# Performance work log

Measured on AMD Instinct MI355X. Metric: run time of the kernel, lower is better.

## Reference

```python
import jax, jax.numpy as jnp
import numpy as np

N, E, H = 4096, 32768, 8
D0, C1, C2, C3 = 256, 448, 384, 256
K, M, G = 4, 500, 2000
NEG = 0.2   # GATConv LeakyReLU negative slope
EPS = 1e-5  # LayerNorm eps


def _gat(x, src, dst, W, a_s, a_d, b, heads, out_ch, concat):
    # PyG GATConv (self-loops already appended to src/dst by caller).
    n = x.shape[0]
    xp = (x @ W).reshape(n, heads, out_ch)                 # [N,H,C]
    s = jnp.einsum('nhc,hc->nh', xp, a_s)                  # alpha_src per node
    d = jnp.einsum('nhc,hc->nh', xp, a_d)                  # alpha_dst per node
    e = jax.nn.leaky_relu(s[src] + d[dst], NEG)            # [E,H]
    m = jax.ops.segment_max(e, dst, num_segments=n)
    m = jnp.where(jnp.isfinite(m), m, 0.0)
    p = jnp.exp(e - m[dst])
    z = jax.ops.segment_sum(p, dst, num_segments=n)
    alpha = p / (z[dst] + 1e-16)                           # per-dst softmax
    out = jax.ops.segment_sum(alpha[:, :, None] * xp[src], dst, num_segments=n)
    out = out.reshape(n, heads * out_ch) if concat else out[:, 0, :]
    return out + b


def _ln(x, g, b):
    mu = x.mean(-1, keepdims=True)
    v = ((x - mu) ** 2).mean(-1, keepdims=True)
    return (x - mu) * jax.lax.rsqrt(v + EPS) * g + b


def setup_inputs() -> dict:
    key = jax.random.key(0)
    ks = jax.random.split(key, 20)
    sc = 0.05
    inp = {
        'x': jax.random.normal(ks[0], (N, D0), jnp.float32),
        'edge_index': jax.random.randint(ks[1], (2, E), 0, N, jnp.int32),
        'W1': jax.random.normal(ks[2], (D0, H * C1), jnp.float32) * sc,
        'as1': jax.random.normal(ks[3], (H, C1), jnp.float32) * sc,
        'ad1': jax.random.normal(ks[4], (H, C1), jnp.float32) * sc,
        'b1': jnp.zeros((H * C1,), jnp.float32),
        'g1': jnp.ones((H * C1,), jnp.float32),
        'be1': jnp.zeros((H * C1,), jnp.float32),
        'W2': jax.random.normal(ks[5], (H * C1, H * C2), jnp.float32) * sc,
        'as2': jax.random.normal(ks[6], (H, C2), jnp.float32) * sc,
        'ad2': jax.random.normal(ks[7], (H, C2), jnp.float32) * sc,
        'b2': jnp.zeros((H * C2,), jnp.float32),
        'g2': jnp.ones((H * C2,), jnp.float32),
        'be2': jnp.zeros((H * C2,), jnp.float32),
        'W3': jax.random.normal(ks[8], (H * C2, H * C3), jnp.float32) * sc,
        'as3': jax.random.normal(ks[9], (H, C3), jnp.float32) * sc,
        'ad3': jax.random.normal(ks[10], (H, C3), jnp.float32) * sc,
        'b3': jnp.zeros((H * C3,), jnp.float32),
        'g3': jnp.ones((H * C3,), jnp.float32),
        'be3': jnp.zeros((H * C3,), jnp.float32),
        'Wh': jax.random.normal(ks[11], (K, H * C3, M), jnp.float32) * sc,
        'ash': jax.random.normal(ks[12], (K, 1, M), jnp.float32) * sc,
        'adh': jax.random.normal(ks[13], (K, 1, M), jnp.float32) * sc,
        'bh': jnp.zeros((K, M), jnp.float32),
        'idx': jnp.arange(G, dtype=jnp.int32).reshape(K, M),
    }
    return inp


def reference(x, edge_index, W1, as1, ad1, b1, g1, be1, W2, as2, ad2, b2, g2, be2,
              W3, as3, ad3, b3, g3, be3, Wh, ash, adh, bh, idx):
    n = x.shape[0]
    # eval mode: dropout_edge is identity; PyG GATConv adds self-loops
    loops = jnp.arange(n, dtype=edge_index.dtype)
    src = jnp.concatenate([edge_index[0], loops])
    dst = jnp.concatenate([edge_index[1], loops])

    h = jax.nn.relu(_gat(x, src, dst, W1, as1, ad1, b1, H, C1, True))
    h = _ln(h, g1, be1)
    h = jax.nn.relu(_gat(h, src, dst, W2, as2, ad2, b2, H, C2, True))
    h = _ln(h, g2, be2)
    h = jax.nn.relu(_gat(h, src, dst, W3, as3, ad3, b3, H, C3, True))
    h = _ln(h, g3, be3)

    per_head = jax.vmap(
        lambda Wk, ak_s, ak_d, bk: _gat(h, src, dst, Wk, ak_s, ak_d, bk, 1, M, False)
    )(Wh, ash, adh, bh)                                    # [K,N,M]

    vals = per_head.transpose(1, 0, 2).reshape(n, K * M)   # [N, G] in head order
    full = jnp.zeros((n, G), vals.dtype).at[:, idx.reshape(-1)].set(vals)
    return full, per_head
```

## Files before the change

kernel.cpp:

```cpp
#include <hip/hip_runtime.h>

#define NN 4096
#define EE 32768
#define ETOT (EE + NN)
#define HH 8
#define KK 4
#define MM 500
#define GG 2000
#define NEGS 0.2f
#define LNEPS 1e-5f

typedef unsigned short ushort;
typedef _Float16 half_t;
typedef __attribute__((ext_vector_type(8))) _Float16 half8;
typedef __attribute__((ext_vector_type(4))) float floatx4;


__device__ __forceinline__ void get_edge(const int* __restrict__ ei, int e, int& s, int& d) {
    if (e < EE) { s = ei[e]; d = ei[EE + e]; }
    else        { s = e - EE; d = e - EE; }
}

__device__ __forceinline__ half_t f2h(float x) { return (half_t)x; }

__device__ __forceinline__ void async_lds16(const half_t* g, half_t* l) {
    __builtin_amdgcn_global_load_lds(
        (const __attribute__((address_space(1))) unsigned int*)(const void*)g,
        (__attribute__((address_space(3))) unsigned int*)(void*)l,
        16, 0, 0);
}


__global__ void k_zero_i(int* p, int n) {
    int i = blockIdx.x * 256 + threadIdx.x;
    if (i < n) p[i] = 0;
}

__global__ void k_count(const int* __restrict__ ei, int* deg) {
    int e = blockIdx.x * 256 + threadIdx.x;
    if (e < ETOT) { int s, d; get_edge(ei, e, s, d); atomicAdd(&deg[d], 1); }
}

__global__ void k_scan(const int* __restrict__ deg, int* rs, int n) {
    __shared__ int sums[1024];
    int tid = threadIdx.x;
    int base = tid * 4;
    int loc[4]; int s = 0;
    #pragma unroll
    for (int i = 0; i < 4; i++) {
        int v = (base + i < n) ? deg[base + i] : 0;
        loc[i] = s; s += v;
    }
    sums[tid] = s;
    __syncthreads();
    for (int off = 1; off < 1024; off <<= 1) {
        int v = (tid >= off) ? sums[tid - off] : 0;
        __syncthreads();
        sums[tid] += v;
        __syncthreads();
    }
    int prev = (tid > 0) ? sums[tid - 1] : 0;
    #pragma unroll
    for (int i = 0; i < 4; i++)
        if (base + i < n) rs[base + i] = prev + loc[i];
    if (tid == 1023) rs[n] = sums[1023];
}

__global__ void k_fill(const int* __restrict__ ei, const int* __restrict__ rs,
                       int* cur, int* csr_src, int* csr_eid) {
    int e = blockIdx.x * 256 + threadIdx.x;
    if (e < ETOT) {
        int s, d; get_edge(ei, e, s, d);
        int pos = rs[d] + atomicAdd(&cur[d], 1);
        csr_src[pos] = s;
        csr_eid[pos] = e;
    }
}


__global__ void k_f2h(const float* __restrict__ in, half_t* __restrict__ out, int n) {
    int i = blockIdx.x * 256 + threadIdx.x;
    if (i < n) out[i] = f2h(in[i]);
}


__global__ __launch_bounds__(256) void k_wt(const float* __restrict__ W,
                                            half_t* __restrict__ Wt,
                                            int Kd, int Nvalid, int ldw,
                                            long long sW, long long sWt) {
    __shared__ float t[32][33];
    const float* Wp = W + (size_t)blockIdx.z * sW;
    half_t* Wtp = Wt + (size_t)blockIdx.z * sWt;
    int n0 = blockIdx.x * 32, k0 = blockIdx.y * 32;
    int tx = threadIdx.x & 31, ty = threadIdx.x >> 5;
    #pragma unroll
    for (int i = 0; i < 32; i += 8)
        t[ty + i][tx] = (n0 + tx < Nvalid) ? Wp[(size_t)(k0 + ty + i) * ldw + n0 + tx] : 0.f;
    __syncthreads();
    #pragma unroll
    for (int i = 0; i < 32; i += 8)
        Wtp[(size_t)(n0 + ty + i) * Kd + k0 + tx] = f2h(t[tx][ty + i]);
}


#define BM 128
#define BN 128
#define BK 64

__global__ __launch_bounds__(256) void k_gemm_mfma(
    const half_t* __restrict__ A,
    const half_t* __restrict__ Bt,
    half_t* __restrict__ C,
    int Kd, int Nreal, int ldc,
    long long strideBt, long long strideC)
{
    __shared__ __align__(16) half_t As[BM * BK];
    __shared__ __align__(16) half_t Bs[BN * BK];

    const half_t* Btp = Bt + (size_t)blockIdx.z * strideBt;
    half_t* Cp = C + (size_t)blockIdx.z * strideC;
    int col0 = blockIdx.x * BN, row0 = blockIdx.y * BM;

    int lane = threadIdx.x & 63;
    int wave = threadIdx.x >> 6;
    int wm = (wave >> 1) * 64, wn = (wave & 1) * 64;

    int srow = wave * 32 + (lane >> 3);
    int gchunk = (lane & 7) ^ ((lane >> 3) & 7);
    const half_t* ga = A   + (size_t)(row0 + srow) * Kd + gchunk * 8;
    const half_t* gb = Btp + (size_t)(col0 + srow) * Kd + gchunk * 8;
    half_t* lA = &As[(wave * 32) * BK];
    half_t* lB = &Bs[(wave * 32) * BK];

    int r = lane & 15;
    int rx = r & 7;

    floatx4 acc[4][4];
    #pragma unroll
    for (int i = 0; i < 4; i++)
        #pragma unroll
        for (int j = 0; j < 4; j++) acc[i][j] = (floatx4){0.f, 0.f, 0.f, 0.f};

    for (int k0 = 0; k0 < Kd; k0 += BK) {
        #pragma unroll
        for (int j = 0; j < 4; j++) {
            async_lds16(ga + k0 + (size_t)(j * 8) * Kd, lA + (j * 8) * BK);
            async_lds16(gb + k0 + (size_t)(j * 8) * Kd, lB + (j * 8) * BK);
        }
        __syncthreads();
        #pragma unroll
        for (int kk = 0; kk < BK; kk += 32) {
            int phys = (((kk >> 3) + (lane >> 4)) ^ rx) << 3;
            half8 a[4], b[4];
            #pragma unroll
            for (int i = 0; i < 4; i++)
                a[i] = *(const half8*)&As[(wm + i * 16 + r) * BK + phys];
            #pragma unroll
            for (int j = 0; j < 4; j++)
                b[j] = *(const half8*)&Bs[(wn + j * 16 + r) * BK + phys];
            #pragma unroll
            for (int i = 0; i < 4; i++)
                #pragma unroll
                for (int j = 0; j < 4; j++)
                    acc[i][j] = __builtin_amdgcn_mfma_f32_16x16x32_f16(a[i], b[j], acc[i][j], 0, 0, 0);
        }
        __syncthreads();
    }

    int q4 = (lane >> 4) * 4;
    #pragma unroll
    for (int i = 0; i < 4; i++) {
        #pragma unroll
        for (int rr = 0; rr < 4; rr++) {
            int row = row0 + wm + i * 16 + q4 + rr;
            #pragma unroll
            for (int j = 0; j < 4; j++) {
                int col = col0 + wn + j * 16 + (lane & 15);
                if (col < Nreal) Cp[(size_t)row * ldc + col] = f2h(acc[i][j][rr]);
            }
        }
    }
}


__global__ void k_sd(const half_t* __restrict__ xp, const float* __restrict__ as_,
                     const float* __restrict__ ad_, float* s, float* d, float* z,
                     int H, int C) {
    int n = blockIdx.x / H, h = blockIdx.x % H;
    int lane = threadIdx.x;
    const half_t* row = xp + (size_t)n * H * C + (size_t)h * C;
    const float* av = as_ + (size_t)h * C;
    const float* bv = ad_ + (size_t)h * C;
    float ss = 0.f, dd = 0.f;
    for (int c = lane; c < C; c += 64) {
        float x = (float)row[c];
        ss += x * av[c];
        dd += x * bv[c];
    }
    #pragma unroll
    for (int o = 32; o > 0; o >>= 1) {
        ss += __shfl_down(ss, o, 64);
        dd += __shfl_down(dd, o, 64);
    }
    if (lane == 0) { s[n * H + h] = ss; d[n * H + h] = dd; z[n * H + h] = 0.f; }
}


__global__ void k_edge(const int* __restrict__ ei, const float* __restrict__ s,
                       const float* __restrict__ d, float* ew, float* z,
                       int H, int total) {
    int i = blockIdx.x * 256 + threadIdx.x;
    if (i >= total) return;
    int e = i / H, h = i - e * H;
    int sn, dn; get_edge(ei, e, sn, dn);
    float v = s[sn * H + h] + d[dn * H + h];
    v = (v >= 0.f) ? v : NEGS * v;
    float p = expf(v);
    ew[i] = p;
    atomicAdd(&z[dn * H + h], p);
}


__global__ __launch_bounds__(256) void k_agg_ln(
    const half_t* __restrict__ xp, const float* __restrict__ p, const float* __restrict__ z,
    const int* __restrict__ csr_src, const int* __restrict__ csr_eid,
    const int* __restrict__ rs, const float* __restrict__ bias,
    const float* __restrict__ gam, const float* __restrict__ bet,
    half_t* __restrict__ outh, int H, int C) {
    __shared__ int sh_src[256];
    __shared__ int sh_eid[256];
    __shared__ float sh_w[256 * HH];
    __shared__ float red[256];
    __shared__ float red2[256];
    int n = blockIdx.x, tid = threadIdx.x;
    int Dout = H * C;
    int NCH = Dout >> 3;
    int CCH = C >> 3;
    int start = rs[n], end = rs[n + 1];
    float acc[2][8];
    #pragma unroll
    for (int a = 0; a < 2; a++)
        #pragma unroll
        for (int e = 0; e < 8; e++) acc[a][e] = 0.f;

    for (int e0 = start; e0 < end; e0 += 256) {
        int cnt = min(256, end - e0);
        if (tid < cnt) { sh_src[tid] = csr_src[e0 + tid]; sh_eid[tid] = csr_eid[e0 + tid]; }
        __syncthreads();
        for (int i = tid; i < cnt * H; i += 256)
            sh_w[i] = p[sh_eid[i / H] * H + (i % H)];
        __syncthreads();
        int ai = 0;
        for (int ch = tid; ch < NCH; ch += 256, ai++) {
            int h = ch / CCH;
            float a0 = acc[ai][0], a1 = acc[ai][1], a2 = acc[ai][2], a3 = acc[ai][3];
            float a4 = acc[ai][4], a5 = acc[ai][5], a6 = acc[ai][6], a7 = acc[ai][7];
            for (int i = 0; i < cnt; i++) {
                float w = sh_w[i * H + h];
                half8 v = *(const half8*)(xp + (size_t)sh_src[i] * Dout + (ch << 3));
                a0 += w * (float)v[0]; a1 += w * (float)v[1];
                a2 += w * (float)v[2]; a3 += w * (float)v[3];
                a4 += w * (float)v[4]; a5 += w * (float)v[5];
                a6 += w * (float)v[6]; a7 += w * (float)v[7];
            }
            acc[ai][0] = a0; acc[ai][1] = a1; acc[ai][2] = a2; acc[ai][3] = a3;
            acc[ai][4] = a4; acc[ai][5] = a5; acc[ai][6] = a6; acc[ai][7] = a7;
        }
        __syncthreads();
    }

    float vals[2][8];
    float sum = 0.f, sumsq = 0.f;
    int ai = 0;
    for (int ch = tid; ch < NCH; ch += 256, ai++) {
        int h = ch / CCH;
        float zi = 1.f / (z[n * H + h] + 1e-16f);
        #pragma unroll
        for (int e = 0; e < 8; e++) {
            float v = acc[ai][e] * zi + bias[(ch << 3) + e];
            v = fmaxf(v, 0.f);
            vals[ai][e] = v;
            sum += v; sumsq += v * v;
        }
    }
    red[tid] = sum; red2[tid] = sumsq;
    __syncthreads();
    for (int o = 128; o > 0; o >>= 1) {
        if (tid < o) { red[tid] += red[tid + o]; red2[tid] += red2[tid + o]; }
        __syncthreads();
    }
    float mu = red[0] / Dout;
    float var = red2[0] / Dout - mu * mu;
    float rstd = rsqrtf(var + LNEPS);
    ai = 0;
    for (int ch = tid; ch < NCH; ch += 256, ai++) {
        half8 o;
        #pragma unroll
        for (int e = 0; e < 8; e++)
            o[e] = f2h((vals[ai][e] - mu) * rstd * gam[(ch << 3) + e] + bet[(ch << 3) + e]);
        *(half8*)(outh + (size_t)n * Dout + (ch << 3)) = o;
    }
}


__global__ __launch_bounds__(256) void k_agg_head(
    const half_t* __restrict__ xp, const float* __restrict__ p, const float* __restrict__ z,
    const int* __restrict__ csr_src, const int* __restrict__ csr_eid,
    const int* __restrict__ rs, const float* __restrict__ bias,
    const int* __restrict__ idxm, float* out_full, float* out_ph) {
    __shared__ int sh_src[256];
    __shared__ int sh_eid[256];
    __shared__ float sh_w[256 * KK];
    int n = blockIdx.x, tid = threadIdx.x;
    const int Dout = KK * MM;
    const int NCH = Dout >> 3;
    int start = rs[n], end = rs[n + 1];
    float acc[8];
    #pragma unroll
    for (int e = 0; e < 8; e++) acc[e] = 0.f;
    int ch = tid;
    int cb = ch << 3;

    for (int e0 = start; e0 < end; e0 += 256) {
        int cnt = min(256, end - e0);
        if (tid < cnt) { sh_src[tid] = csr_src[e0 + tid]; sh_eid[tid] = csr_eid[e0 + tid]; }
        __syncthreads();
        for (int i = tid; i < cnt * KK; i += 256)
            sh_w[i] = p[sh_eid[i / KK] * KK + (i % KK)];
        __syncthreads();
        if (ch < NCH) {
            for (int i = 0; i < cnt; i++) {
                const float* wv = &sh_w[i * KK];
                half8 v = *(const half8*)(xp + (size_t)sh_src[i] * Dout + cb);
                #pragma unroll
                for (int e = 0; e < 8; e++)
                    acc[e] += wv[(cb + e) / MM] * (float)v[e];
            }
        }
        __syncthreads();
    }
    if (ch < NCH) {
        #pragma unroll
        for (int e = 0; e < 8; e++) {
            int c = cb + e;
            int k = c / MM, m = c - k * MM;
            float v = acc[e] / (z[n * KK + k] + 1e-16f) + bias[c];
            out_ph[((size_t)k * NN + n) * MM + m] = v;
            out_full[(size_t)n * GG + idxm[c]] = v;
        }
    }
}


extern "C" void kernel_launch(void* const* d_in, const int* in_sizes, int n_in,
                              void* d_out, int out_size, void* d_ws, size_t ws_size,
                              hipStream_t stream) {
    (void)in_sizes; (void)n_in; (void)out_size; (void)ws_size;
    const float* x   = (const float*)d_in[0];
    const int*   ei  = (const int*)d_in[1];
    const float* W1  = (const float*)d_in[2];
    const float* as1 = (const float*)d_in[3];
    const float* ad1 = (const float*)d_in[4];
    const float* b1  = (const float*)d_in[5];
    const float* g1  = (const float*)d_in[6];
    const float* be1 = (const float*)d_in[7];
    const float* W2  = (const float*)d_in[8];
    const float* as2 = (const float*)d_in[9];
    const float* ad2 = (const float*)d_in[10];
    const float* b2  = (const float*)d_in[11];
    const float* g2  = (const float*)d_in[12];
    const float* be2 = (const float*)d_in[13];
    const float* W3  = (const float*)d_in[14];
    const float* as3 = (const float*)d_in[15];
    const float* ad3 = (const float*)d_in[16];
    const float* b3  = (const float*)d_in[17];
    const float* g3  = (const float*)d_in[18];
    const float* be3 = (const float*)d_in[19];
    const float* Wh  = (const float*)d_in[20];
    const float* ash = (const float*)d_in[21];
    const float* adh = (const float*)d_in[22];
    const float* bh  = (const float*)d_in[23];
    const int*   idxm = (const int*)d_in[24];
    float* out = (float*)d_out;

    char* w = (char*)d_ws;
    auto carve = [&](size_t bytes) { char* p = w; w += (bytes + 255) & ~(size_t)255; return p; };
    half_t* xp16    = (half_t*)carve((size_t)NN * 3584 * 2);
    half_t* Wt      = (half_t*)carve((size_t)3072 * 3584 * 2);
    float*  sarr    = (float*)carve((size_t)NN * HH * 4);
    float*  darr    = (float*)carve((size_t)NN * HH * 4);
    float*  zarr    = (float*)carve((size_t)NN * HH * 4);
    float*  ework   = (float*)carve((size_t)ETOT * HH * 4);
    int*    csr_src = (int*)carve((size_t)ETOT * 4);
    int*    csr_eid = (int*)carve((size_t)ETOT * 4);
    int*    rowst   = (int*)carve((size_t)(NN + 1) * 4);
    int*    cur     = (int*)carve((size_t)NN * 4);
    half_t* Ah = (half_t*)d_out;

    k_zero_i<<<(NN + 255) / 256, 256, 0, stream>>>(cur, NN);
    k_count<<<(ETOT + 255) / 256, 256, 0, stream>>>(ei, cur);
    k_scan<<<1, 1024, 0, stream>>>(cur, rowst, NN);
    k_zero_i<<<(NN + 255) / 256, 256, 0, stream>>>(cur, NN);
    k_fill<<<(ETOT + 255) / 256, 256, 0, stream>>>(ei, rowst, cur, csr_src, csr_eid);

    k_f2h<<<(NN * 256 + 255) / 256, 256, 0, stream>>>(x, Ah, NN * 256);

    auto gat = [&](const float* W, const float* as_, const float* ad_,
                   const float* bias, const float* gam, const float* bet, int Din, int C) {
        int Dout = HH * C;
        k_wt<<<dim3(Dout / 32, Din / 32, 1), 256, 0, stream>>>(W, Wt, Din, Dout, Dout, 0, 0);
        k_gemm_mfma<<<dim3(Dout / BN, NN / BM, 1), 256, 0, stream>>>(
            Ah, Wt, xp16, Din, Dout, Dout, 0, 0);
        k_sd<<<NN * HH, 64, 0, stream>>>(xp16, as_, ad_, sarr, darr, zarr, HH, C);
        int tot = ETOT * HH;
        k_edge<<<(tot + 255) / 256, 256, 0, stream>>>(ei, sarr, darr, ework, zarr, HH, tot);
        k_agg_ln<<<NN, 256, 0, stream>>>(xp16, ework, zarr, csr_src, csr_eid, rowst,
                                         bias, gam, bet, Ah, HH, C);
    };
    gat(W1, as1, ad1, b1, g1, be1, 256,  448);
    gat(W2, as2, ad2, b2, g2, be2, 3584, 384);
    gat(W3, as3, ad3, b3, g3, be3, 3072, 256);

    k_wt<<<dim3(512 / 32, 2048 / 32, KK), 256, 0, stream>>>(
        Wh, Wt, 2048, MM, MM, (long long)2048 * MM, (long long)512 * 2048);
    k_gemm_mfma<<<dim3(512 / BN, NN / BM, KK), 256, 0, stream>>>(
        Ah, Wt, xp16, 2048, MM, GG, (long long)512 * 2048, (long long)MM);
    k_sd<<<NN * KK, 64, 0, stream>>>(xp16, ash, adh, sarr, darr, zarr, KK, MM);
    int tot = ETOT * KK;
    k_edge<<<(tot + 255) / 256, 256, 0, stream>>>(ei, sarr, darr, ework, zarr, KK, tot);
    k_agg_head<<<NN, 256, 0, stream>>>(xp16, ework, zarr, csr_src, csr_eid, rowst,
                                       bh, idxm, out, out + (size_t)NN * GG);
}
```

Baseline: 674.7 us.

## Fuse edge softmax weight computation into aggregation kernels, drop k_edge

The separate edge kernel, which computed exp(leaky_relu(s+d)) per edge and head, wrote an edge weight buffer and atomically accumulated the softmax denominator, is removed. Each aggregation block now recomputes its incoming edges' weights from the s/d arrays straight into shared memory and sums the denominator locally. This removes four kernel launches, the edge-weight buffer round trip, the global atomics and the csr_eid indirection. The cost is a few redundant exp evaluations and a serial per-head denominator sum in each block.

```diff
diff --git a/kernel.cpp b/kernel.cpp
--- a/kernel.cpp
+++ b/kernel.cpp
@@ -67,13 +67,12 @@
 }
 
 __global__ void k_fill(const int* __restrict__ ei, const int* __restrict__ rs,
-                       int* cur, int* csr_src, int* csr_eid) {
+                       int* cur, int* csr_src) {
     int e = blockIdx.x * 256 + threadIdx.x;
     if (e < ETOT) {
         int s, d; get_edge(ei, e, s, d);
         int pos = rs[d] + atomicAdd(&cur[d], 1);
         csr_src[pos] = s;
-        csr_eid[pos] = e;
     }
 }
 
@@ -184,8 +183,7 @@
 
 
 __global__ void k_sd(const half_t* __restrict__ xp, const float* __restrict__ as_,
-                     const float* __restrict__ ad_, float* s, float* d, float* z,
-                     int H, int C) {
+                     const float* __restrict__ ad_, float* s, float* d, int H, int C) {
     int n = blockIdx.x / H, h = blockIdx.x % H;
     int lane = threadIdx.x;
     const half_t* row = xp + (size_t)n * H * C + (size_t)h * C;
@@ -202,34 +200,19 @@
         ss += __shfl_down(ss, o, 64);
         dd += __shfl_down(dd, o, 64);
     }
-    if (lane == 0) { s[n * H + h] = ss; d[n * H + h] = dd; z[n * H + h] = 0.f; }
-}
-
-
-__global__ void k_edge(const int* __restrict__ ei, const float* __restrict__ s,
-                       const float* __restrict__ d, float* ew, float* z,
-                       int H, int total) {
-    int i = blockIdx.x * 256 + threadIdx.x;
-    if (i >= total) return;
-    int e = i / H, h = i - e * H;
-    int sn, dn; get_edge(ei, e, sn, dn);
-    float v = s[sn * H + h] + d[dn * H + h];
-    v = (v >= 0.f) ? v : NEGS * v;
-    float p = expf(v);
-    ew[i] = p;
-    atomicAdd(&z[dn * H + h], p);
+    if (lane == 0) { s[n * H + h] = ss; d[n * H + h] = dd; }
 }
 
 
 __global__ __launch_bounds__(256) void k_agg_ln(
-    const half_t* __restrict__ xp, const float* __restrict__ p, const float* __restrict__ z,
-    const int* __restrict__ csr_src, const int* __restrict__ csr_eid,
-    const int* __restrict__ rs, const float* __restrict__ bias,
-    const float* __restrict__ gam, const float* __restrict__ bet,
-    half_t* __restrict__ outh, int H, int C) {
+    const half_t* __restrict__ xp, const float* __restrict__ s, const float* __restrict__ d,
+    const int* __restrict__ csr_src, const int* __restrict__ rs,
+    const float* __restrict__ bias, const float* __restrict__ gam,
+    const float* __restrict__ bet, half_t* __restrict__ outh, int H, int C) {
     __shared__ int sh_src[256];
-    __shared__ int sh_eid[256];
     __shared__ float sh_w[256 * HH];
+    __shared__ float sh_d[HH];
+    __shared__ float sh_z[HH];
     __shared__ float red[256];
     __shared__ float red2[256];
     int n = blockIdx.x, tid = threadIdx.x;
@@ -237,6 +220,7 @@
     int NCH = Dout >> 3;
     int CCH = C >> 3;
     int start = rs[n], end = rs[n + 1];
+    if (tid < H) { sh_d[tid] = d[(size_t)n * H + tid]; sh_z[tid] = 0.f; }
     float acc[2][8];
     #pragma unroll
     for (int a = 0; a < 2; a++)
@@ -245,11 +229,20 @@
 
     for (int e0 = start; e0 < end; e0 += 256) {
         int cnt = min(256, end - e0);
-        if (tid < cnt) { sh_src[tid] = csr_src[e0 + tid]; sh_eid[tid] = csr_eid[e0 + tid]; }
-        __syncthreads();
-        for (int i = tid; i < cnt * H; i += 256)
-            sh_w[i] = p[sh_eid[i / H] * H + (i % H)];
-        __syncthreads();
+        if (tid < cnt) sh_src[tid] = csr_src[e0 + tid];
+        __syncthreads();
+        for (int i = tid; i < cnt * H; i += 256) {
+            int ei = i / H, h = i - ei * H;
+            float v = s[(size_t)sh_src[ei] * H + h] + sh_d[h];
+            v = (v >= 0.f) ? v : NEGS * v;
+            sh_w[i] = expf(v);
+        }
+        __syncthreads();
+        if (tid < H) {
+            float zz = 0.f;
+            for (int i = 0; i < cnt; i++) zz += sh_w[i * H + tid];
+            sh_z[tid] += zz;
+        }
         int ai = 0;
         for (int ch = tid; ch < NCH; ch += 256, ai++) {
             int h = ch / CCH;
@@ -274,7 +267,7 @@
     int ai = 0;
     for (int ch = tid; ch < NCH; ch += 256, ai++) {
         int h = ch / CCH;
-        float zi = 1.f / (z[n * H + h] + 1e-16f);
+        float zi = 1.f / (sh_z[h] + 1e-16f);
         #pragma unroll
         for (int e = 0; e < 8; e++) {
             float v = acc[ai][e] * zi + bias[(ch << 3) + e];
@@ -304,17 +297,19 @@
 
 
 __global__ __launch_bounds__(256) void k_agg_head(
-    const half_t* __restrict__ xp, const float* __restrict__ p, const float* __restrict__ z,
-    const int* __restrict__ csr_src, const int* __restrict__ csr_eid,
-    const int* __restrict__ rs, const float* __restrict__ bias,
-    const int* __restrict__ idxm, float* out_full, float* out_ph) {
+    const half_t* __restrict__ xp, const float* __restrict__ s, const float* __restrict__ d,
+    const int* __restrict__ csr_src, const int* __restrict__ rs,
+    const float* __restrict__ bias, const int* __restrict__ idxm,
+    float* out_full, float* out_ph) {
     __shared__ int sh_src[256];
-    __shared__ int sh_eid[256];
     __shared__ float sh_w[256 * KK];
+    __shared__ float sh_d[KK];
+    __shared__ float sh_z[KK];
     int n = blockIdx.x, tid = threadIdx.x;
     const int Dout = KK * MM;
     const int NCH = Dout >> 3;
     int start = rs[n], end = rs[n + 1];
+    if (tid < KK) { sh_d[tid] = d[(size_t)n * KK + tid]; sh_z[tid] = 0.f; }
     float acc[8];
     #pragma unroll
     for (int e = 0; e < 8; e++) acc[e] = 0.f;
@@ -323,11 +318,20 @@
 
     for (int e0 = start; e0 < end; e0 += 256) {
         int cnt = min(256, end - e0);
-        if (tid < cnt) { sh_src[tid] = csr_src[e0 + tid]; sh_eid[tid] = csr_eid[e0 + tid]; }
-        __syncthreads();
-        for (int i = tid; i < cnt * KK; i += 256)
-            sh_w[i] = p[sh_eid[i / KK] * KK + (i % KK)];
-        __syncthreads();
+        if (tid < cnt) sh_src[tid] = csr_src[e0 + tid];
+        __syncthreads();
+        for (int i = tid; i < cnt * KK; i += 256) {
+            int ei = i / KK, k = i - ei * KK;
+            float v = s[(size_t)sh_src[ei] * KK + k] + sh_d[k];
+            v = (v >= 0.f) ? v : NEGS * v;
+            sh_w[i] = expf(v);
+        }
+        __syncthreads();
+        if (tid < KK) {
+            float zz = 0.f;
+            for (int i = 0; i < cnt; i++) zz += sh_w[i * KK + tid];
+            sh_z[tid] += zz;
+        }
         if (ch < NCH) {
             for (int i = 0; i < cnt; i++) {
                 const float* wv = &sh_w[i * KK];
@@ -344,7 +348,7 @@
         for (int e = 0; e < 8; e++) {
             int c = cb + e;
             int k = c / MM, m = c - k * MM;
-            float v = acc[e] / (z[n * KK + k] + 1e-16f) + bias[c];
+            float v = acc[e] / (sh_z[k] + 1e-16f) + bias[c];
             out_ph[((size_t)k * NN + n) * MM + m] = v;
             out_full[(size_t)n * GG + idxm[c]] = v;
         }
@@ -389,10 +393,7 @@
     half_t* Wt      = (half_t*)carve((size_t)3072 * 3584 * 2);
     float*  sarr    = (float*)carve((size_t)NN * HH * 4);
     float*  darr    = (float*)carve((size_t)NN * HH * 4);
-    float*  zarr    = (float*)carve((size_t)NN * HH * 4);
-    float*  ework   = (float*)carve((size_t)ETOT * HH * 4);
     int*    csr_src = (int*)carve((size_t)ETOT * 4);
-    int*    csr_eid = (int*)carve((size_t)ETOT * 4);
     int*    rowst   = (int*)carve((size_t)(NN + 1) * 4);
     int*    cur     = (int*)carve((size_t)NN * 4);
     half_t* Ah = (half_t*)d_out;
@@ -401,7 +402,7 @@
     k_count<<<(ETOT + 255) / 256, 256, 0, stream>>>(ei, cur);
     k_scan<<<1, 1024, 0, stream>>>(cur, rowst, NN);
     k_zero_i<<<(NN + 255) / 256, 256, 0, stream>>>(cur, NN);
-    k_fill<<<(ETOT + 255) / 256, 256, 0, stream>>>(ei, rowst, cur, csr_src, csr_eid);
+    k_fill<<<(ETOT + 255) / 256, 256, 0, stream>>>(ei, rowst, cur, csr_src);
 
     k_f2h<<<(NN * 256 + 255) / 256, 256, 0, stream>>>(x, Ah, NN * 256);
 
@@ -411,10 +412,8 @@
         k_wt<<<dim3(Dout / 32, Din / 32, 1), 256, 0, stream>>>(W, Wt, Din, Dout, Dout, 0, 0);
         k_gemm_mfma<<<dim3(Dout / BN, NN / BM, 1), 256, 0, stream>>>(
             Ah, Wt, xp16, Din, Dout, Dout, 0, 0);
-        k_sd<<<NN * HH, 64, 0, stream>>>(xp16, as_, ad_, sarr, darr, zarr, HH, C);
-        int tot = ETOT * HH;
-        k_edge<<<(tot + 255) / 256, 256, 0, stream>>>(ei, sarr, darr, ework, zarr, HH, tot);
-        k_agg_ln<<<NN, 256, 0, stream>>>(xp16, ework, zarr, csr_src, csr_eid, rowst,
+        k_sd<<<NN * HH, 64, 0, stream>>>(xp16, as_, ad_, sarr, darr, HH, C);
+        k_agg_ln<<<NN, 256, 0, stream>>>(xp16, sarr, darr, csr_src, rowst,
                                          bias, gam, bet, Ah, HH, C);
     };
     gat(W1, as1, ad1, b1, g1, be1, 256,  448);
@@ -425,9 +424,7 @@
         Wh, Wt, 2048, MM, MM, (long long)2048 * MM, (long long)512 * 2048);
     k_gemm_mfma<<<dim3(512 / BN, NN / BM, KK), 256, 0, stream>>>(
         Ah, Wt, xp16, 2048, MM, GG, (long long)512 * 2048, (long long)MM);
-    k_sd<<<NN * KK, 64, 0, stream>>>(xp16, ash, adh, sarr, darr, zarr, KK, MM);
-    int tot = ETOT * KK;
-    k_edge<<<(tot + 255) / 256, 256, 0, stream>>>(ei, sarr, darr, ework, zarr, KK, tot);
-    k_agg_head<<<NN, 256, 0, stream>>>(xp16, ework, zarr, csr_src, csr_eid, rowst,
+    k_sd<<<NN * KK, 64, 0, stream>>>(xp16, ash, adh, sarr, darr, KK, MM);
+    k_agg_head<<<NN, 256, 0, stream>>>(xp16, sarr, darr, csr_src, rowst,
                                        bh, idxm, out, out + (size_t)NN * GG);
 }
```

New measurement: 697.1 us. 3.3% more time.
